# Optimization experiments

Hardware: AMD Instinct MI355X
Metric: run time of the kernel (lower is better)

The kernel has to match this reference:

```python
import jax, jax.numpy as jnp
import numpy as np

N = 4096
C = 64
B = 4
DIST_THRESHOLD = 0.5
ALPHA = 0.01
NEG_INF = -1e15


def setup_inputs() -> dict:
    key = jax.random.key(0)
    k1, k2, k3, k4, k5 = jax.random.split(key, 5)
    x = jax.random.normal(k1, (B, N, C), dtype=jnp.float32)
    dist_mat = jax.random.uniform(k2, (N, N), dtype=jnp.float32)
    proj_w = jax.random.normal(k3, (N, C, C), dtype=jnp.float32) / np.sqrt(C)
    proj_b = jax.random.normal(k4, (N, C), dtype=jnp.float32) * 0.01
    a_w = jax.random.normal(k5, (N, 2 * C), dtype=jnp.float32) / np.sqrt(2 * C)
    return {"x": x, "dist_mat": dist_mat, "proj_w": proj_w, "proj_b": proj_b, "a_w": a_w}


def reference(x, dist_mat, proj_w, proj_b, a_w):
    # Adjacency: (0 < dist < threshold), diagonal forced to 1.
    adj = (dist_mat > 0) & (dist_mat < DIST_THRESHOLD)
    adj = adj | jnp.eye(N, dtype=bool)

    # Per-node projection (GraphDense): h[b,n,:] = x[b,n,:] @ proj_w[n] + proj_b[n]
    h = jnp.einsum('bnc,nco->bno', x, proj_w) + proj_b  # [B, N, C]

    # Attention score: a[j] . concat(h_i, h_j) without materializing [B,N,N,2C].
    a_src, a_dst = a_w[:, :C], a_w[:, C:]               # each [N, C]
    s = jnp.einsum('bic,jc->bij', h, a_src) + jnp.einsum('bjc,jc->bj', h, a_dst)[:, None, :]
    s = jnp.where(s >= 0, s, ALPHA * s)                 # LeakyReLU
    s = jnp.where(adj[None, :, :], s, NEG_INF)          # mask non-edges
    att = jax.nn.softmax(s, axis=-1)                    # [B, N, N]

    # Weighted aggregation over neighbors.
    y = jnp.einsum('bij,bjc->bic', att, h)              # [B, N, C]
    return y
```

## Files before the change

kernel.cpp:

```cpp
#include <hip/hip_runtime.h>

#define N 4096
#define C 64
#define B 4

typedef __attribute__((ext_vector_type(8))) short short8;
typedef __attribute__((ext_vector_type(4))) float f32x4;

#define MFMA16(a, b, c) __builtin_amdgcn_mfma_f32_16x16x32_bf16(a, b, c, 0, 0, 0)

__device__ __forceinline__ short f2bf(float f) {
    unsigned u = __builtin_bit_cast(unsigned, f);
    u += 0x7fffu + ((u >> 16) & 1u);
    return (short)(u >> 16);
}

__global__ __launch_bounds__(256) void proj_kernel(
    const float* __restrict__ x,
    const float* __restrict__ proj_w,
    const float* __restrict__ proj_b,
    const float* __restrict__ a_w,
    short* __restrict__ h_bf,
    short* __restrict__ hT_bf,
    short* __restrict__ a_srcb,
    float* __restrict__ e2)
{
    __shared__ float lds_x[B][C];
    __shared__ float lds_acc[4][B][C];

    const int tid = threadIdx.x;
    const int wave = tid >> 6;
    const int lane = tid & 63;
    const int n = blockIdx.x;

    lds_x[wave][lane] = x[((size_t)wave * N + n) * C + lane];
    __syncthreads();

    const int o4 = (lane & 15) * 4;
    const int cl = lane >> 4;
    const float* Wn = proj_w + (size_t)n * C * C;

    float4 acc[B];
#pragma unroll
    for (int b = 0; b < B; b++) acc[b] = make_float4(0.f, 0.f, 0.f, 0.f);

#pragma unroll
    for (int i = 0; i < 4; i++) {
        int c = wave * 16 + i * 4 + cl;
        float4 wv = *(const float4*)(Wn + c * C + o4);
#pragma unroll
        for (int b = 0; b < B; b++) {
            float xc = lds_x[b][c];
            acc[b].x = fmaf(xc, wv.x, acc[b].x);
            acc[b].y = fmaf(xc, wv.y, acc[b].y);
            acc[b].z = fmaf(xc, wv.z, acc[b].z);
            acc[b].w = fmaf(xc, wv.w, acc[b].w);
        }
    }
#pragma unroll
    for (int b = 0; b < B; b++) {
#pragma unroll
        for (int off = 16; off < 64; off <<= 1) {
            acc[b].x += __shfl_xor(acc[b].x, off, 64);
            acc[b].y += __shfl_xor(acc[b].y, off, 64);
            acc[b].z += __shfl_xor(acc[b].z, off, 64);
            acc[b].w += __shfl_xor(acc[b].w, off, 64);
        }
        if (lane < 16) *(float4*)(&lds_acc[wave][b][o4]) = acc[b];
    }
    __syncthreads();

    {
        const int b = wave, o = lane;
        float hval = proj_b[(size_t)n * C + o] + lds_acc[0][b][o] + lds_acc[1][b][o] +
                     lds_acc[2][b][o] + lds_acc[3][b][o];
        float adst = a_w[(size_t)n * (2 * C) + C + o];
        short hb = f2bf(hval);
        h_bf[((size_t)b * N + n) * C + o] = hb;
        hT_bf[(size_t)b * C * N + (size_t)o * N + n] = hb;
        float prod = hval * adst;
#pragma unroll
        for (int off = 32; off; off >>= 1) prod += __shfl_xor(prod, off, 64);
        if (lane == 0) e2[b * N + n] = prod;
        if (tid < C) a_srcb[(size_t)n * C + tid] = f2bf(a_w[(size_t)n * (2 * C) + tid]);
    }
}

__global__ __launch_bounds__(256) void attn_kernel(
    const float* __restrict__ dist,
    const short* __restrict__ h_bf,
    const short* __restrict__ hT_bf,
    const short* __restrict__ a_srcb,
    const float* __restrict__ e2,
    float* __restrict__ part_y,
    float* __restrict__ part_m,
    float* __restrict__ part_l,
    int JS, int mode)
{
    __shared__ float lds_dist[16 * 68];
    __shared__ short lds_p[4][16 * 72];

    const int tid = threadIdx.x;
    const int wave = tid >> 6;
    const int lane = tid & 63;
    const int cl = lane & 15;
    const int rg = lane >> 4;
    const int b = wave;
    const int i0 = blockIdx.x * 16;
    const int sidx = blockIdx.y;
    const int jbeg = sidx * JS;

    const short* hrow = h_bf + ((size_t)b * N + i0 + cl) * C;
    short8 af0 = *(const short8*)(hrow + rg * 8);
    short8 af1 = *(const short8*)(hrow + 32 + rg * 8);

    f32x4 yacc[4];
#pragma unroll
    for (int t = 0; t < 4; t++) { f32x4 z = {0.f, 0.f, 0.f, 0.f}; yacc[t] = z; }
    float mrow[4] = {-1e30f, -1e30f, -1e30f, -1e30f};
    float lrow[4] = {0.f, 0.f, 0.f, 0.f};

    for (int j0 = jbeg; j0 < jbeg + JS; j0 += 64) {
        __syncthreads();
        {
            int r = tid >> 4;
            int cc = (tid & 15) * 4;
            *(float4*)(&lds_dist[r * 68 + cc]) =
                *(const float4*)(dist + (size_t)(i0 + r) * N + j0 + cc);
        }
        __syncthreads();

        f32x4 sacc[4];
#pragma unroll
        for (int t = 0; t < 4; t++) {
            f32x4 z = {0.f, 0.f, 0.f, 0.f};
            const short* arow = a_srcb + (size_t)(j0 + t * 16 + cl) * C + rg * 8;
            short8 b0 = *(const short8*)(arow);
            short8 b1 = *(const short8*)(arow + 32);
            z = MFMA16(af0, b0, z);
            z = MFMA16(af1, b1, z);
            sacc[t] = z;
        }

        float e2v[4];
#pragma unroll
        for (int t = 0; t < 4; t++) e2v[t] = e2[b * N + j0 + t * 16 + cl];

        float p[4][4];
        float mcur[4] = {-1e30f, -1e30f, -1e30f, -1e30f};
#pragma unroll
        for (int t = 0; t < 4; t++) {
#pragma unroll
            for (int r = 0; r < 4; r++) {
                float sv = sacc[t][r] + e2v[t];
                sv = (sv >= 0.f) ? sv : 0.01f * sv;
                int row = rg * 4 + r;
                float d = lds_dist[row * 68 + t * 16 + cl];
                bool adj = (d > 0.f && d < 0.5f) || (i0 + row == j0 + t * 16 + cl);
                sv = adj ? sv : -1e15f;
                p[t][r] = sv;
                mcur[r] = fmaxf(mcur[r], sv);
            }
        }

        float alpha[4];
#pragma unroll
        for (int r = 0; r < 4; r++) {
            float mx = mcur[r];
#pragma unroll
            for (int off = 8; off; off >>= 1) mx = fmaxf(mx, __shfl_xor(mx, off, 64));
            float mnew = fmaxf(mrow[r], mx);
            alpha[r] = __expf(mrow[r] - mnew);
            mrow[r] = mnew;
            float ps = 0.f;
#pragma unroll
            for (int t = 0; t < 4; t++) {
                float pv = __expf(p[t][r] - mnew);
                p[t][r] = pv;
                ps += pv;
            }
#pragma unroll
            for (int off = 8; off; off >>= 1) ps += __shfl_xor(ps, off, 64);
            lrow[r] = lrow[r] * alpha[r] + ps;
        }

#pragma unroll
        for (int t = 0; t < 4; t++)
#pragma unroll
            for (int r = 0; r < 4; r++) yacc[t][r] *= alpha[r];

        short* lp = lds_p[wave];
#pragma unroll
        for (int t = 0; t < 4; t++)
#pragma unroll
            for (int r = 0; r < 4; r++)
                lp[(rg * 4 + r) * 72 + t * 16 + cl] = f2bf(p[t][r]);
        short8 pa0 = *(const short8*)(lp + cl * 72 + rg * 8);
        short8 pa1 = *(const short8*)(lp + cl * 72 + 32 + rg * 8);

#pragma unroll
        for (int t = 0; t < 4; t++) {
            const short* hc = hT_bf + (size_t)b * C * N + (size_t)(t * 16 + cl) * N + j0 + rg * 8;
            short8 h0 = *(const short8*)(hc);
            short8 h1 = *(const short8*)(hc + 32);
            yacc[t] = MFMA16(pa0, h0, yacc[t]);
            yacc[t] = MFMA16(pa1, h1, yacc[t]);
        }
    }

    if (mode) {
#pragma unroll
        for (int t = 0; t < 4; t++)
#pragma unroll
            for (int r = 0; r < 4; r++)
                part_y[((size_t)b * N + i0 + rg * 4 + r) * C + t * 16 + cl] =
                    yacc[t][r] / lrow[r];
    } else {
        size_t sb = (size_t)(sidx * B + b) * N;
#pragma unroll
        for (int t = 0; t < 4; t++)
#pragma unroll
            for (int r = 0; r < 4; r++)
                part_y[(sb + i0 + rg * 4 + r) * C + t * 16 + cl] = yacc[t][r];
        if (cl == 0) {
#pragma unroll
            for (int r = 0; r < 4; r++) {
                part_m[sb + i0 + rg * 4 + r] = mrow[r];
                part_l[sb + i0 + rg * 4 + r] = lrow[r];
            }
        }
    }
}

__global__ __launch_bounds__(256) void combine_kernel(
    const float* __restrict__ part_y, const float* __restrict__ part_m,
    const float* __restrict__ part_l, float* __restrict__ out, int S)
{
    int g = blockIdx.x * 256 + threadIdx.x;
    int c = g & 63;
    int row = (g >> 6) & (N - 1);
    int b = g >> 18;
    int bn = b * N + row;
    float m = -1e30f;
    for (int s = 0; s < S; s++) m = fmaxf(m, part_m[s * (B * N) + bn]);
    float l = 0.f, y = 0.f;
    for (int s = 0; s < S; s++) {
        float w = __expf(part_m[s * (B * N) + bn] - m);
        l += part_l[s * (B * N) + bn] * w;
        y += part_y[((size_t)s * B * N + bn) * C + c] * w;
    }
    out[g] = y / l;
}

extern "C" void kernel_launch(void* const* d_in, const int* in_sizes, int n_in,
                              void* d_out, int out_size, void* d_ws, size_t ws_size,
                              hipStream_t stream) {
    const float* x      = (const float*)d_in[0];
    const float* dist   = (const float*)d_in[1];
    const float* proj_w = (const float*)d_in[2];
    const float* proj_b = (const float*)d_in[3];
    const float* a_w    = (const float*)d_in[4];
    float* out = (float*)d_out;

    char* ws = (char*)d_ws;
    short* h_bf   = (short*)(ws);
    short* hT_bf  = (short*)(ws + (2u << 20));
    short* a_srcb = (short*)(ws + (4u << 20));
    float* e2     = (float*)(ws + (4u << 20) + (512u << 10));
    float* part_m = (float*)(ws + (5u << 20));
    float* part_l = (float*)(ws + (5u << 20) + (512u << 10));
    float* part_y = (float*)(ws + (6u << 20));

    proj_kernel<<<N, 256, 0, stream>>>(x, proj_w, proj_b, a_w, h_bf, hT_bf, a_srcb, e2);

    int S = 8;
    while (S > 1 && (6u << 20) + (size_t)S * B * N * C * 4 > ws_size) S >>= 1;
    bool direct = ((6u << 20) + (size_t)B * N * C * 4 > ws_size);

    if (direct) {
        attn_kernel<<<dim3(N / 16, 1), 256, 0, stream>>>(
            dist, h_bf, hT_bf, a_srcb, e2, out, part_m, part_l, N, 1);
    } else {
        attn_kernel<<<dim3(N / 16, S), 256, 0, stream>>>(
            dist, h_bf, hT_bf, a_srcb, e2, part_y, part_m, part_l, N / S, 0);
        combine_kernel<<<(B * N * C) / 256, 256, 0, stream>>>(part_y, part_m, part_l, out, S);
    }
}
```

Baseline: 286.9 us.

## Precompute adjacency bitmask, add coalesced transpose kernel, stage e2 in LDS

A new mask kernel turns the dense float distance matrix into a 64-bit-per-64-column adjacency bitmask using wave ballots. The attention kernel then reads a few u64 words per tile instead of staging float distances through LDS, which also removes two block barriers per iteration. The strided scattered transpose writes in the projection kernel are replaced by a separate LDS-tiled transpose kernel, and the e2 values are preloaded into LDS when the j-slice is small enough. The cost is two extra kernel launches and one full pass over dist_mat that is not overlapped with other work.

```diff
diff --git a/kernel.cpp b/kernel.cpp
--- a/kernel.cpp
+++ b/kernel.cpp
@@ -6,6 +6,7 @@
 
 typedef __attribute__((ext_vector_type(8))) short short8;
 typedef __attribute__((ext_vector_type(4))) float f32x4;
+typedef unsigned long long u64;
 
 #define MFMA16(a, b, c) __builtin_amdgcn_mfma_f32_16x16x32_bf16(a, b, c, 0, 0, 0)
 
@@ -13,6 +14,21 @@
     unsigned u = __builtin_bit_cast(unsigned, f);
     u += 0x7fffu + ((u >> 16) & 1u);
     return (short)(u >> 16);
+}
+
+__global__ __launch_bounds__(256) void mask_kernel(const float* __restrict__ dist,
+                                                   u64* __restrict__ msk) {
+    const int wave = threadIdx.x >> 6, lane = threadIdx.x & 63;
+    const int i = blockIdx.x * 4 + wave;
+    const float* row = dist + (size_t)i * N;
+#pragma unroll 4
+    for (int jb = 0; jb < N / 64; jb++) {
+        float d = row[jb * 64 + lane];
+        u64 m = __ballot(d > 0.f && d < 0.5f);
+        int dj = i - jb * 64;
+        if (dj >= 0 && dj < 64) m |= (1ull << dj);
+        if (lane == 0) msk[(size_t)i * (N / 64) + jb] = m;
+    }
 }
 
 __global__ __launch_bounds__(256) void proj_kernel(
@@ -21,7 +37,6 @@
     const float* __restrict__ proj_b,
     const float* __restrict__ a_w,
     short* __restrict__ h_bf,
-    short* __restrict__ hT_bf,
     short* __restrict__ a_srcb,
     float* __restrict__ e2)
 {
@@ -75,9 +90,7 @@
         float hval = proj_b[(size_t)n * C + o] + lds_acc[0][b][o] + lds_acc[1][b][o] +
                      lds_acc[2][b][o] + lds_acc[3][b][o];
         float adst = a_w[(size_t)n * (2 * C) + C + o];
-        short hb = f2bf(hval);
-        h_bf[((size_t)b * N + n) * C + o] = hb;
-        hT_bf[(size_t)b * C * N + (size_t)o * N + n] = hb;
+        h_bf[((size_t)b * N + n) * C + o] = f2bf(hval);
         float prod = hval * adst;
 #pragma unroll
         for (int off = 32; off; off >>= 1) prod += __shfl_xor(prod, off, 64);
@@ -86,8 +99,33 @@
     }
 }
 
+__global__ __launch_bounds__(256) void transpose_kernel(const short* __restrict__ h_bf,
+                                                        short* __restrict__ hT_bf) {
+    __shared__ short tile[64][72];
+    const int t = threadIdx.x;
+    const int b = blockIdx.y;
+    const int n0 = blockIdx.x * 64;
+    {
+        int r = t >> 2, cs = (t & 3) * 16;
+        const short* src = h_bf + ((size_t)b * N + n0 + r) * C + cs;
+#pragma unroll
+        for (int q = 0; q < 4; q++)
+            *(short4*)&tile[r][cs + q * 4] = *(const short4*)(src + q * 4);
+    }
+    __syncthreads();
+    {
+        int c = t >> 2, ns = (t & 3) * 16;
+        short v[16];
+#pragma unroll
+        for (int k = 0; k < 16; k++) v[k] = tile[ns + k][c];
+        short* dst = hT_bf + (size_t)b * C * N + (size_t)c * N + n0 + ns;
+        *(short8*)dst = *(short8*)&v[0];
+        *(short8*)(dst + 8) = *(short8*)&v[8];
+    }
+}
+
 __global__ __launch_bounds__(256) void attn_kernel(
-    const float* __restrict__ dist,
+    const u64* __restrict__ msk,
     const short* __restrict__ h_bf,
     const short* __restrict__ hT_bf,
     const short* __restrict__ a_srcb,
@@ -97,8 +135,8 @@
     float* __restrict__ part_l,
     int JS, int mode)
 {
-    __shared__ float lds_dist[16 * 68];
     __shared__ short lds_p[4][16 * 72];
+    __shared__ float lds_e2[4][512];
 
     const int tid = threadIdx.x;
     const int wave = tid >> 6;
@@ -107,13 +145,23 @@
     const int rg = lane >> 4;
     const int b = wave;
     const int i0 = blockIdx.x * 16;
-    const int sidx = blockIdx.y;
-    const int jbeg = sidx * JS;
+    const int jbeg = blockIdx.y * JS;
+    const bool e2lds = (JS <= 512);
+
+    if (e2lds) {
+        for (int q = lane * 4; q < JS; q += 256)
+            *(float4*)&lds_e2[wave][q] = *(const float4*)(e2 + (size_t)b * N + jbeg + q);
+    }
 
     const short* hrow = h_bf + ((size_t)b * N + i0 + cl) * C;
     short8 af0 = *(const short8*)(hrow + rg * 8);
     short8 af1 = *(const short8*)(hrow + 32 + rg * 8);
 
+    const u64* mrow_base[4];
+#pragma unroll
+    for (int r = 0; r < 4; r++)
+        mrow_base[r] = msk + (size_t)(i0 + rg * 4 + r) * (N / 64);
+
     f32x4 yacc[4];
 #pragma unroll
     for (int t = 0; t < 4; t++) { f32x4 z = {0.f, 0.f, 0.f, 0.f}; yacc[t] = z; }
@@ -121,14 +169,14 @@
     float lrow[4] = {0.f, 0.f, 0.f, 0.f};
 
     for (int j0 = jbeg; j0 < jbeg + JS; j0 += 64) {
-        __syncthreads();
-        {
-            int r = tid >> 4;
-            int cc = (tid & 15) * 4;
-            *(float4*)(&lds_dist[r * 68 + cc]) =
-                *(const float4*)(dist + (size_t)(i0 + r) * N + j0 + cc);
-        }
-        __syncthreads();
+        const int jb = j0 >> 6;
+        unsigned mlo[4], mhi[4];
+#pragma unroll
+        for (int r = 0; r < 4; r++) {
+            u64 m = mrow_base[r][jb];
+            mlo[r] = (unsigned)m;
+            mhi[r] = (unsigned)(m >> 32);
+        }
 
         f32x4 sacc[4];
 #pragma unroll
@@ -144,7 +192,9 @@
 
         float e2v[4];
 #pragma unroll
-        for (int t = 0; t < 4; t++) e2v[t] = e2[b * N + j0 + t * 16 + cl];
+        for (int t = 0; t < 4; t++)
+            e2v[t] = e2lds ? lds_e2[wave][j0 - jbeg + t * 16 + cl]
+                           : e2[(size_t)b * N + j0 + t * 16 + cl];
 
         float p[4][4];
         float mcur[4] = {-1e30f, -1e30f, -1e30f, -1e30f};
@@ -154,9 +204,8 @@
             for (int r = 0; r < 4; r++) {
                 float sv = sacc[t][r] + e2v[t];
                 sv = (sv >= 0.f) ? sv : 0.01f * sv;
-                int row = rg * 4 + r;
-                float d = lds_dist[row * 68 + t * 16 + cl];
-                bool adj = (d > 0.f && d < 0.5f) || (i0 + row == j0 + t * 16 + cl);
+                unsigned bits = (t < 2) ? mlo[r] : mhi[r];
+                bool adj = (bits >> ((t & 1) * 16 + cl)) & 1u;
                 sv = adj ? sv : -1e15f;
                 p[t][r] = sv;
                 mcur[r] = fmaxf(mcur[r], sv);
@@ -216,7 +265,7 @@
                 part_y[((size_t)b * N + i0 + rg * 4 + r) * C + t * 16 + cl] =
                     yacc[t][r] / lrow[r];
     } else {
-        size_t sb = (size_t)(sidx * B + b) * N;
+        size_t sb = (size_t)(blockIdx.y * B + b) * N;
 #pragma unroll
         for (int t = 0; t < 4; t++)
 #pragma unroll
@@ -267,22 +316,25 @@
     short* hT_bf  = (short*)(ws + (2u << 20));
     short* a_srcb = (short*)(ws + (4u << 20));
     float* e2     = (float*)(ws + (4u << 20) + (512u << 10));
-    float* part_m = (float*)(ws + (5u << 20));
-    float* part_l = (float*)(ws + (5u << 20) + (512u << 10));
-    float* part_y = (float*)(ws + (6u << 20));
-
-    proj_kernel<<<N, 256, 0, stream>>>(x, proj_w, proj_b, a_w, h_bf, hT_bf, a_srcb, e2);
+    u64*   msk    = (u64*)  (ws + (5u << 20));
+    float* part_m = (float*)(ws + (7u << 20));
+    float* part_l = (float*)(ws + (7u << 20) + (512u << 10));
+    float* part_y = (float*)(ws + (8u << 20));
+
+    proj_kernel<<<N, 256, 0, stream>>>(x, proj_w, proj_b, a_w, h_bf, a_srcb, e2);
+    transpose_kernel<<<dim3(N / 64, B), 256, 0, stream>>>(h_bf, hT_bf);
+    mask_kernel<<<N / 4, 256, 0, stream>>>(dist, msk);
 
     int S = 8;
-    while (S > 1 && (6u << 20) + (size_t)S * B * N * C * 4 > ws_size) S >>= 1;
-    bool direct = ((6u << 20) + (size_t)B * N * C * 4 > ws_size);
+    while (S > 1 && (8u << 20) + (size_t)S * B * N * C * 4 > ws_size) S >>= 1;
+    bool direct = ((8u << 20) + (size_t)B * N * C * 4 > ws_size);
 
     if (direct) {
         attn_kernel<<<dim3(N / 16, 1), 256, 0, stream>>>(
-            dist, h_bf, hT_bf, a_srcb, e2, out, part_m, part_l, N, 1);
+            msk, h_bf, hT_bf, a_srcb, e2, out, part_m, part_l, N, 1);
     } else {
         attn_kernel<<<dim3(N / 16, S), 256, 0, stream>>>(
-            dist, h_bf, hT_bf, a_srcb, e2, part_y, part_m, part_l, N / S, 0);
+            msk, h_bf, hT_bf, a_srcb, e2, part_y, part_m, part_l, N / S, 0);
         combine_kernel<<<(B * N * C) / 256, 256, 0, stream>>>(part_y, part_m, part_l, out, S);
     }
 }
```

After: 331.1 us. 1.15x slower.
